# Optimization experiments

Hardware: AMD Instinct MI355X
Metric: run time of the kernel (lower is better)

Reference implementation:

```python
import jax, jax.numpy as jnp
import numpy as np

B, L, T = 32, 256, 32
V_SIZE, D, H = 30000, 300, 256


def _gru(x, h0, Wih, Whh, bih, bhh):
    # x: [B,S,D], h0: [B,H]; PyTorch GRU gate order: r, z, n
    xg = jnp.einsum('bsd,gd->bsg', x, Wih) + bih  # [B,S,3H]

    def step(h, xg_t):
        gh = jnp.einsum('bh,gh->bg', h, Whh) + bhh
        ir, iz, in_ = jnp.split(xg_t, 3, axis=-1)
        hr, hz, hn_ = jnp.split(gh, 3, axis=-1)
        r = jax.nn.sigmoid(ir + hr)
        z = jax.nn.sigmoid(iz + hz)
        n = jnp.tanh(in_ + r * hn_)
        h_new = (1.0 - z) * n + z * h
        return h_new, h_new

    h_last, outs = jax.lax.scan(step, h0, jnp.swapaxes(xg, 0, 1))
    return jnp.swapaxes(outs, 0, 1), h_last  # [B,S,H], [B,H]


def setup_inputs() -> dict:
    rng = np.random.default_rng(0)
    Xin = rng.integers(0, V_SIZE, (B, L)).astype(np.int64)
    # strictly increasing segment ends; starts = previous end + 1
    Yindex = np.stack([np.sort(rng.choice(L, T, replace=False)) for _ in range(B)]).astype(np.int64)
    Xindex = np.concatenate([np.zeros((B, 1), np.int64), Yindex[:, :-1] + 1], axis=1)
    lens = np.full((B,), L, np.int64)
    s = 0.05
    p = lambda *shape: jnp.asarray(rng.standard_normal(shape) * s, jnp.float32)
    return {
        'Xin': jnp.asarray(Xin), 'Xindex': jnp.asarray(Xindex),
        'Yindex': jnp.asarray(Yindex), 'lens': jnp.asarray(lens),
        'emb': jnp.asarray(rng.standard_normal((V_SIZE, D)) * 0.1, jnp.float32),
        'Wih_e': p(3 * H, D), 'Whh_e': p(3 * H, H), 'bih_e': p(3 * H), 'bhh_e': p(3 * H),
        'Wih_d': p(3 * H, D), 'Whh_d': p(3 * H, H), 'bih_d': p(3 * H), 'bhh_d': p(3 * H),
        'W1': p(H, H), 'W2': p(H, H), 'Vv': p(H),
    }


def reference(Xin, Xindex, Yindex, lens, emb, Wih_e, Whh_e, bih_e, bhh_e,
              Wih_d, Whh_d, bih_d, bhh_d, W1, W2, Vv):
    # pointerEncoder (isbanor=False, dropout=0, lens==L so packed == plain)
    X = emb[Xin]                                   # [B,L,D]
    h0 = jnp.zeros((Xin.shape[0], Whh_e.shape[1]), X.dtype)
    hn, h_end = _gru(X, h0, Wih_e, Whh_e, bih_e, bhh_e)  # [B,L,H],[B,H]
    # training_decoder, vectorized over batch and decode steps
    dec_tok = jnp.take_along_axis(Xin, Xindex, axis=1)   # token ids at segment starts
    dx = emb[dec_tok]                              # [B,T,D]
    dout, _ = _gru(dx, h_end, Wih_d, Whh_d, bih_d, bhh_d)  # [B,T,H]
    # pointerLayer: v = selu(V . selu(W1 en + W2 d)), masked log_softmax over [start, curL)
    WE = jnp.einsum('blh,kh->blk', hn, W1)         # [B,L,H]
    WD = jnp.einsum('bth,kh->btk', dout, W2)       # [B,T,H]
    s = jax.nn.selu(WE[:, None, :, :] + WD[:, :, None, :])  # [B,T,L,H]
    v = jax.nn.selu(jnp.einsum('btlh,h->btl', s, Vv))        # [B,T,L]
    pos = jnp.arange(hn.shape[1])
    mask = (pos[None, None, :] >= Xindex[:, :, None]) & (pos[None, None, :] < lens[:, None, None])
    logits = jnp.where(mask, v, -jnp.inf)
    logp = jax.nn.log_softmax(logits, axis=-1)
    tgt_logp = jnp.take_along_axis(logp, Yindex[:, :, None], axis=-1)[..., 0]  # [B,T]
    return -jnp.mean(tgt_logp)  # batch_loss / LoopN
```

## Files before the change

### kernel.cpp

```cpp
#include <hip/hip_runtime.h>
#include <hip/hip_bf16.h>
#include <stdint.h>

#define B_  32
#define L_  256
#define T_  32
#define D_  300
#define H_  256
#define G3  768

__device__ __forceinline__ int sdot4(uint32_t a, uint32_t b, int acc) {
#if defined(__has_builtin) && __has_builtin(__builtin_amdgcn_sdot4)
  return __builtin_amdgcn_sdot4((int)a, (int)b, acc, false);
#else
  const int a0 = (int)(signed char)(a & 0xff),  b0 = (int)(signed char)(b & 0xff);
  const int a1 = (int)(signed char)((a >> 8) & 0xff),  b1 = (int)(signed char)((b >> 8) & 0xff);
  const int a2 = (int)(signed char)((a >> 16) & 0xff), b2 = (int)(signed char)((b >> 16) & 0xff);
  const int a3 = (int)(signed char)(a >> 24),          b3 = (int)(signed char)(b >> 24);
  return acc + a0 * b0 + a1 * b1 + a2 * b2 + a3 * b3;
#endif
}

__device__ __forceinline__ float rcp_f(float x) { return __builtin_amdgcn_rcpf(x); }
__device__ __forceinline__ float sigmoid_f(float x) { return rcp_f(1.0f + __expf(-x)); }
__device__ __forceinline__ float tanh_f(float x) {
  float e2 = __expf(2.0f * x);
  return 1.0f - 2.0f * rcp_f(e2 + 1.0f);
}

__global__ __launch_bounds__(256)
void pack_whh_i8(const float* __restrict__ Whh, uint32_t* __restrict__ wQ,
                 float* __restrict__ sw) {
  const int row = blockIdx.x * 4 + (threadIdx.x >> 6);
  const int lane = threadIdx.x & 63;
  const float* wr = Whh + (long)row * H_;
  float m = 0.0f;
#pragma unroll
  for (int u = 0; u < 4; ++u) m = fmaxf(m, fabsf(wr[lane + 64 * u]));
  for (int off = 32; off > 0; off >>= 1) m = fmaxf(m, __shfl_xor(m, off, 64));
  const float inv = m > 0.0f ? 127.0f / m : 0.0f;
  if (lane == 0) sw[row] = m > 0.0f ? m / (127.0f * 127.0f) : 0.0f;
  uint32_t d = 0;
#pragma unroll
  for (int u = 0; u < 4; ++u) {
    int qv = __float2int_rn(wr[4 * lane + u] * inv);
    qv = qv > 127 ? 127 : (qv < -127 ? -127 : qv);
    d |= ((uint32_t)(qv & 0xff)) << (8 * u);
  }
  wQ[(((size_t)(lane >> 2) * G3 + row) << 2) + (lane & 3)] = d;
}

__global__ __launch_bounds__(256)
void quant_rows(const float* __restrict__ A, const int* __restrict__ rowidx,
                uint32_t* __restrict__ out, float* __restrict__ scale,
                int M, int K, int Kd) {
  const int row = blockIdx.x * 4 + (threadIdx.x >> 6);
  const int lane = threadIdx.x & 63;
  if (row >= M) return;
  const float* ar = A + (long)(rowidx ? rowidx[row] : row) * K;
  float m = 0.0f;
  for (int e = lane; e < K; e += 64) m = fmaxf(m, fabsf(ar[e]));
  for (int off = 32; off > 0; off >>= 1) m = fmaxf(m, __shfl_xor(m, off, 64));
  const float inv = m > 0.0f ? 127.0f / m : 0.0f;
  if (lane == 0) scale[row] = m * (1.0f / 127.0f);
  for (int kd = lane; kd < Kd; kd += 64) {
    uint32_t d = 0;
#pragma unroll
    for (int u = 0; u < 4; ++u) {
      const int e = 4 * kd + u;
      int qv = (e < K) ? __float2int_rn(ar[e] * inv) : 0;
      qv = qv > 127 ? 127 : (qv < -127 ? -127 : qv);
      d |= ((uint32_t)(qv & 0xff)) << (8 * u);
    }
    out[(long)row * Kd + kd] = d;
  }
}

__global__ void bias_combine(const float* __restrict__ bih, const float* __restrict__ bhh,
                             float* __restrict__ bsum) {
  const int i = blockIdx.x * 256 + threadIdx.x;
  float v = bih[i];
  if (i < 2 * H_) v += bhh[i];
  bsum[i] = v;
}

__global__ void gather_dtok(const int* __restrict__ Xin, const int* __restrict__ Xindex,
                            int* __restrict__ dtok) {
  const int i = blockIdx.x * 256 + threadIdx.x;
  const int b = i >> 5;
  dtok[i] = Xin[b * L_ + Xindex[i]];
}

template<bool TRANSP, bool BIAS>
__global__ __launch_bounds__(256)
void gemm_i8(const uint32_t* __restrict__ Aq, const float* __restrict__ sa,
             const uint32_t* __restrict__ Wq, const float* __restrict__ swc,
             const float* __restrict__ bias, float* __restrict__ C,
             int M, int N, int Kd) {
  __shared__ uint32_t As[8][68];
  __shared__ uint32_t Ws[8][68];
  const int tid = threadIdx.x;
  const int bm = blockIdx.x, bn = blockIdx.y;
  const int ty = tid >> 4, tx = tid & 15;
  const int srow = tid >> 2;
  const int skd = (tid & 3) << 1;
  const uint32_t* Arow = Aq + (long)(bm * 64 + srow) * Kd + skd;
  const uint32_t* Wrow = Wq + (long)(bn * 64 + srow) * Kd + skd;
  int acc[4][4] = {};
  for (int k0 = 0; k0 < Kd; k0 += 8) {
    const uint32_t a0 = Arow[k0], a1 = Arow[k0 + 1];
    const uint32_t w0 = Wrow[k0], w1 = Wrow[k0 + 1];
    __syncthreads();
    As[skd][srow] = a0; As[skd + 1][srow] = a1;
    Ws[skd][srow] = w0; Ws[skd + 1][srow] = w1;
    __syncthreads();
#pragma unroll
    for (int kd = 0; kd < 8; ++kd) {
      const uint4 a4 = *(const uint4*)&As[kd][ty << 2];
      const uint4 b4 = *(const uint4*)&Ws[kd][tx << 2];
      acc[0][0] = sdot4(a4.x, b4.x, acc[0][0]);
      acc[0][1] = sdot4(a4.x, b4.y, acc[0][1]);
      acc[0][2] = sdot4(a4.x, b4.z, acc[0][2]);
      acc[0][3] = sdot4(a4.x, b4.w, acc[0][3]);
      acc[1][0] = sdot4(a4.y, b4.x, acc[1][0]);
      acc[1][1] = sdot4(a4.y, b4.y, acc[1][1]);
      acc[1][2] = sdot4(a4.y, b4.z, acc[1][2]);
      acc[1][3] = sdot4(a4.y, b4.w, acc[1][3]);
      acc[2][0] = sdot4(a4.z, b4.x, acc[2][0]);
      acc[2][1] = sdot4(a4.z, b4.y, acc[2][1]);
      acc[2][2] = sdot4(a4.z, b4.z, acc[2][2]);
      acc[2][3] = sdot4(a4.z, b4.w, acc[2][3]);
      acc[3][0] = sdot4(a4.w, b4.x, acc[3][0]);
      acc[3][1] = sdot4(a4.w, b4.y, acc[3][1]);
      acc[3][2] = sdot4(a4.w, b4.z, acc[3][2]);
      acc[3][3] = sdot4(a4.w, b4.w, acc[3][3]);
    }
  }
#pragma unroll
  for (int i = 0; i < 4; ++i) {
    const int m = bm * 64 + (ty << 2) + i;
    const float sai = sa[m];
#pragma unroll
    for (int j = 0; j < 4; ++j) {
      const int n = bn * 64 + (tx << 2) + j;
      float v = (float)acc[i][j] * sai * swc[n];
      if (BIAS) v += bias[n];
      if (TRANSP) C[(((long)(m >> 8) * N + n) << 8) + (m & 255)] = v;
      else        C[(long)m * N + n] = v;
    }
  }
}


#define PIN4(v) asm volatile("" : "+v"(v.x), "+v"(v.y), "+v"(v.z), "+v"(v.w))
#define DOT4W(accv, wv, hp) { \
  accv = sdot4(wv.x, hp.x, accv); accv = sdot4(wv.y, hp.y, accv); \
  accv = sdot4(wv.z, hp.z, accv); accv = sdot4(wv.w, hp.w, accv); }

__global__ __launch_bounds__(1024)
void gru_seq(const float* __restrict__ xg, const uint4* __restrict__ wQv,
             const float* __restrict__ sw, const float* __restrict__ bhh,
             const float* __restrict__ h0, float* __restrict__ hout,
             float* __restrict__ hlast, int S) {
  const int b = blockIdx.x;
  const int tid = threadIdx.x;
  const int j = tid & 255;
  const int q = tid >> 8;
  const int c0 = q * 4;
  const int o_r0 = (c0 + 0) * G3 + j,        o_r1 = (c0 + 1) * G3 + j;
  const int o_z0 = o_r0 + H_,                o_z1 = o_r1 + H_;
  const int o_n0 = o_r0 + 2 * H_,            o_n1 = o_r1 + 2 * H_;
  uint4 wr2 = wQv[(c0 + 2) * G3 + j],          wr3 = wQv[(c0 + 3) * G3 + j];
  uint4 wz2 = wQv[(c0 + 2) * G3 + H_ + j],     wz3 = wQv[(c0 + 3) * G3 + H_ + j];
  uint4 wn2 = wQv[(c0 + 2) * G3 + 2 * H_ + j], wn3 = wQv[(c0 + 3) * G3 + 2 * H_ + j];
  PIN4(wr2); PIN4(wr3); PIN4(wz2); PIN4(wz3); PIN4(wn2); PIN4(wn3);
  __shared__ __align__(16) uint32_t h2[2][H_ / 4];
  __shared__ int part[3][4][H_];
  float bhn = 0.0f, h = 0.0f, swr = 0.0f, swz = 0.0f, swn = 0.0f;
  const float* xp = xg + (long)b * S * G3;
  float* hp_out = hout + (long)b * S * H_;
  if (q == 0) {
    bhn = bhh[2 * H_ + j];
    swr = sw[j]; swz = sw[H_ + j]; swn = sw[2 * H_ + j];
    h = h0 ? h0[b * H_ + j] : 0.0f;
    ((signed char*)h2[0])[j] = (signed char)__float2int_rn(h * 127.0f);
  }
  __syncthreads();
  for (int t = 0; t < S; ++t) {
    const uint4* hq = (const uint4*)h2[t & 1] + q * 4;
    int ar = 0, az = 0, an = 0;
    uint4 s0 = wQv[o_r0], s1 = wQv[o_r1];
    float xr = 0.0f, xz = 0.0f, xn = 0.0f;
    if (q == 0) { xr = xp[j]; xz = xp[H_ + j]; xn = xp[2 * H_ + j]; }
    const uint4 hp2 = hq[2], hp3 = hq[3];
    DOT4W(ar, wr2, hp2) DOT4W(ar, wr3, hp3)
    const uint4 hp0 = hq[0], hp1 = hq[1];
    DOT4W(ar, s0, hp0) DOT4W(ar, s1, hp1)
    __builtin_amdgcn_sched_barrier(0);
    s0 = wQv[o_z0]; s1 = wQv[o_z1];
    DOT4W(az, wz2, hp2) DOT4W(az, wz3, hp3)
    DOT4W(az, s0, hp0) DOT4W(az, s1, hp1)
    __builtin_amdgcn_sched_barrier(0);
    s0 = wQv[o_n0]; s1 = wQv[o_n1];
    DOT4W(an, wn2, hp2) DOT4W(an, wn3, hp3)
    DOT4W(an, s0, hp0) DOT4W(an, s1, hp1)
    if (q) { part[0][q][j] = ar; part[1][q][j] = az; part[2][q][j] = an; }
    __syncthreads();
    if (q == 0) {
      const float arf = (float)(ar + part[0][1][j] + part[0][2][j] + part[0][3][j]) * swr;
      const float azf = (float)(az + part[1][1][j] + part[1][2][j] + part[1][3][j]) * swz;
      const float anf = (float)(an + part[2][1][j] + part[2][2][j] + part[2][3][j]) * swn;
      const float r = sigmoid_f(xr + arf);
      const float z = sigmoid_f(xz + azf);
      const float n = tanh_f(xn + r * (anf + bhn));
      h = (1.0f - z) * n + z * h;
      hp_out[j] = h;
      ((signed char*)h2[(t & 1) ^ 1])[j] = (signed char)__float2int_rn(h * 127.0f);
    }
    xp += G3;
    hp_out += H_;
    __syncthreads();
  }
  if (q == 0 && hlast) hlast[b * H_ + j] = h;
}

__global__ __launch_bounds__(256)
void pointer_loss(const float* __restrict__ WEt, const float* __restrict__ WD,
                  const float* __restrict__ Vv,
                  const int* __restrict__ Xindex, const int* __restrict__ Yindex,
                  const int* __restrict__ lens, float* __restrict__ out) {
  const int t = blockIdx.x, b = blockIdx.y;
  const int l = threadIdx.x;
  __shared__ float wd_s[H_], vv_s[H_];
  __shared__ float rbuf[4], sbuf[4], vy_s;
  const int bt = b * T_ + t;
  wd_s[l] = WD[(long)bt * H_ + l];
  vv_s[l] = Vv[l] * 1.0507009873554805f;
  __syncthreads();
  const float* wet = WEt + (long)b * H_ * L_;
  const float alpha = 1.6732632423543772f;
  float acc = 0.0f;
#pragma unroll 4
  for (int hh = 0; hh < H_; ++hh) {
    const float xsum = wet[hh * L_ + l] + wd_s[hh];
    const float sneg = alpha * (__expf(xsum) - 1.0f);
    const float s = xsum > 0.0f ? xsum : sneg;
    acc = fmaf(s, vv_s[hh], acc);
  }
  float v;
  {
    const float sneg = alpha * (__expf(acc) - 1.0f);
    v = 1.0507009873554805f * (acc > 0.0f ? acc : sneg);
  }
  const int start = Xindex[bt];
  const int len = lens[b];
  const bool valid = (l >= start) && (l < len);
  const int y = Yindex[bt];
  if (l == y) vy_s = v;
  float m = valid ? v : -INFINITY;
  for (int off = 32; off > 0; off >>= 1) m = fmaxf(m, __shfl_xor(m, off, 64));
  const int wid = l >> 6, lane = l & 63;
  if (lane == 0) rbuf[wid] = m;
  __syncthreads();
  const float mx = fmaxf(fmaxf(rbuf[0], rbuf[1]), fmaxf(rbuf[2], rbuf[3]));
  float e = valid ? __expf(v - mx) : 0.0f;
  for (int off = 32; off > 0; off >>= 1) e += __shfl_xor(e, off, 64);
  if (lane == 0) sbuf[wid] = e;
  __syncthreads();
  if (l == 0) {
    const float sum = sbuf[0] + sbuf[1] + sbuf[2] + sbuf[3];
    atomicAdd(out, (mx + __logf(sum) - vy_s) * (1.0f / (B_ * T_)));
  }
}

extern "C" void kernel_launch(void* const* d_in, const int* in_sizes, int n_in,
                              void* d_out, int out_size, void* d_ws, size_t ws_size,
                              hipStream_t stream) {
  (void)in_sizes; (void)n_in; (void)out_size; (void)ws_size;
  const int*   Xin    = (const int*)d_in[0];
  const int*   Xindex = (const int*)d_in[1];
  const int*   Yindex = (const int*)d_in[2];
  const int*   lens   = (const int*)d_in[3];
  const float* emb    = (const float*)d_in[4];
  const float* Wih_e  = (const float*)d_in[5];
  const float* Whh_e  = (const float*)d_in[6];
  const float* bih_e  = (const float*)d_in[7];
  const float* bhh_e  = (const float*)d_in[8];
  const float* Wih_d  = (const float*)d_in[9];
  const float* Whh_d  = (const float*)d_in[10];
  const float* bih_d  = (const float*)d_in[11];
  const float* bhh_d  = (const float*)d_in[12];
  const float* W1     = (const float*)d_in[13];
  const float* W2     = (const float*)d_in[14];
  const float* Vv     = (const float*)d_in[15];

  char* p = (char*)d_ws;
  auto take = [&](size_t bytes) { void* q = (void*)p; p += (bytes + 255) & ~(size_t)255; return q; };
  uint32_t* wQ_e   = (uint32_t*)take((size_t)64 * G3 * 4);
  uint32_t* wQ_d   = (uint32_t*)take((size_t)64 * G3 * 4);
  float*    sw_e   = (float*)take((size_t)768 * 4);
  float*    sw_d   = (float*)take((size_t)768 * 4);
  uint32_t* WihQ_e = (uint32_t*)take((size_t)768 * 80 * 4);
  uint32_t* WihQ_d = (uint32_t*)take((size_t)768 * 80 * 4);
  float*    sWih_e = (float*)take((size_t)768 * 4);
  float*    sWih_d = (float*)take((size_t)768 * 4);
  uint32_t* W1q    = (uint32_t*)take((size_t)256 * 64 * 4);
  uint32_t* W2q    = (uint32_t*)take((size_t)256 * 64 * 4);
  float*    sW1    = (float*)take((size_t)256 * 4);
  float*    sW2    = (float*)take((size_t)256 * 4);
  float*    bsum_e = (float*)take((size_t)768 * 4);
  float*    bsum_d = (float*)take((size_t)768 * 4);
  int*      dtok   = (int*)take((size_t)1024 * 4);
  float*    xg_e   = (float*)take((size_t)8192 * 768 * 4);
  float*    xg_d   = (float*)take((size_t)1024 * 768 * 4);
  float*    hn     = (float*)take((size_t)8192 * 256 * 4);
  float*    hend   = (float*)take((size_t)8192 * 4);
  float*    hl_d   = (float*)take((size_t)8192 * 4);
  float*    doutb  = (float*)take((size_t)1024 * 256 * 4);
  float*    WDb    = (float*)take((size_t)1024 * 256 * 4);
  uint32_t* Aqe    = (uint32_t*)take((size_t)8192 * 80 * 4);
  float*    saAe   = (float*)take((size_t)8192 * 4);
  uint32_t* Aqd    = (uint32_t*)take((size_t)1024 * 80 * 4);
  float*    saAd   = (float*)take((size_t)1024 * 4);
  float*    WEt  = xg_e;
  uint32_t* hnq  = Aqe;
  float*    sahn = saAe;
  uint32_t* dq   = Aqd;
  float*    sad  = saAd;

  hipMemsetAsync(d_out, 0, sizeof(float), stream);

  hipLaunchKernelGGL(pack_whh_i8, dim3(192), dim3(256), 0, stream, Whh_e, wQ_e, sw_e);
  hipLaunchKernelGGL(pack_whh_i8, dim3(192), dim3(256), 0, stream, Whh_d, wQ_d, sw_d);
  hipLaunchKernelGGL(bias_combine, dim3(3), dim3(256), 0, stream, bih_e, bhh_e, bsum_e);
  hipLaunchKernelGGL(bias_combine, dim3(3), dim3(256), 0, stream, bih_d, bhh_d, bsum_d);
  hipLaunchKernelGGL(gather_dtok, dim3(4), dim3(256), 0, stream, Xin, Xindex, dtok);

  hipLaunchKernelGGL(quant_rows, dim3(192), dim3(256), 0, stream,
                     Wih_e, (const int*)nullptr, WihQ_e, sWih_e, 768, 300, 80);
  hipLaunchKernelGGL(quant_rows, dim3(192), dim3(256), 0, stream,
                     Wih_d, (const int*)nullptr, WihQ_d, sWih_d, 768, 300, 80);
  hipLaunchKernelGGL(quant_rows, dim3(64), dim3(256), 0, stream,
                     W1, (const int*)nullptr, W1q, sW1, 256, 256, 64);
  hipLaunchKernelGGL(quant_rows, dim3(64), dim3(256), 0, stream,
                     W2, (const int*)nullptr, W2q, sW2, 256, 256, 64);
  hipLaunchKernelGGL(quant_rows, dim3(2048), dim3(256), 0, stream,
                     emb, Xin, Aqe, saAe, 8192, 300, 80);
  hipLaunchKernelGGL(quant_rows, dim3(256), dim3(256), 0, stream,
                     emb, dtok, Aqd, saAd, 1024, 300, 80);

  hipLaunchKernelGGL((gemm_i8<false, true>), dim3(128, 12), dim3(256), 0, stream,
                     Aqe, saAe, WihQ_e, sWih_e, bsum_e, xg_e, 8192, 768, 80);
  hipLaunchKernelGGL((gemm_i8<false, true>), dim3(16, 12), dim3(256), 0, stream,
                     Aqd, saAd, WihQ_d, sWih_d, bsum_d, xg_d, 1024, 768, 80);

  hipLaunchKernelGGL(gru_seq, dim3(32), dim3(1024), 0, stream,
                     xg_e, (const uint4*)wQ_e, sw_e, bhh_e, (const float*)nullptr,
                     hn, hend, L_);
  hipLaunchKernelGGL(gru_seq, dim3(32), dim3(1024), 0, stream,
                     xg_d, (const uint4*)wQ_d, sw_d, bhh_d, hend, doutb, hl_d, T_);

  hipLaunchKernelGGL(quant_rows, dim3(2048), dim3(256), 0, stream,
                     hn, (const int*)nullptr, hnq, sahn, 8192, 256, 64);
  hipLaunchKernelGGL(quant_rows, dim3(256), dim3(256), 0, stream,
                     doutb, (const int*)nullptr, dq, sad, 1024, 256, 64);
  hipLaunchKernelGGL((gemm_i8<true, false>), dim3(128, 4), dim3(256), 0, stream,
                     hnq, sahn, W1q, sW1, (const float*)nullptr, WEt, 8192, 256, 64);
  hipLaunchKernelGGL((gemm_i8<false, false>), dim3(16, 4), dim3(256), 0, stream,
                     dq, sad, W2q, sW2, (const float*)nullptr, WDb, 1024, 256, 64);

  hipLaunchKernelGGL(pointer_loss, dim3(T_, B_), dim3(256), 0, stream,
                     WEt, WDb, Vv, Xindex, Yindex, lens, (float*)d_out);
}
```

Before: 342.5 us.

## Fuse prep kernels into one launch and broadcast GRU hidden state via readlane

Eleven small preprocessing launches (weight packing, quantization, bias combine, decoder token gather) are merged into one prep_all kernel, and the two post-GRU quantizations into one post_quant kernel, cutting launch overhead and the serialization between tiny kernels. In the recurrent GRU kernel, each thread keeps more of its int8 weights in registers (8 pinned uint4 instead of 6), so fewer weight loads are reissued per step. The hidden state is read once per lane from LDS and broadcast with readlane instead of vector LDS loads, and partial sums are exchanged as one int4 instead of three scalars. The extra pinned registers raise register pressure at 1024 threads per block.

After: 394.2 us. 1.15x slower.

```diff
diff --git a/kernel.cpp b/kernel.cpp
--- a/kernel.cpp
+++ b/kernel.cpp
@@ -28,10 +28,10 @@
   return 1.0f - 2.0f * rcp_f(e2 + 1.0f);
 }
 
-__global__ __launch_bounds__(256)
-void pack_whh_i8(const float* __restrict__ Whh, uint32_t* __restrict__ wQ,
-                 float* __restrict__ sw) {
-  const int row = blockIdx.x * 4 + (threadIdx.x >> 6);
+__device__ __forceinline__ void pack_body(int blk, const float* __restrict__ Whh,
+                                          uint32_t* __restrict__ wQ,
+                                          float* __restrict__ sw) {
+  const int row = blk * 4 + (threadIdx.x >> 6);
   const int lane = threadIdx.x & 63;
   const float* wr = Whh + (long)row * H_;
   float m = 0.0f;
@@ -50,14 +50,20 @@
   wQ[(((size_t)(lane >> 2) * G3 + row) << 2) + (lane & 3)] = d;
 }
 
-__global__ __launch_bounds__(256)
-void quant_rows(const float* __restrict__ A, const int* __restrict__ rowidx,
-                uint32_t* __restrict__ out, float* __restrict__ scale,
-                int M, int K, int Kd) {
-  const int row = blockIdx.x * 4 + (threadIdx.x >> 6);
+__device__ __forceinline__ void quant_body(int blk, const float* __restrict__ A,
+                                           const int* __restrict__ rowidx,
+                                           const int* __restrict__ Xin2,
+                                           const int* __restrict__ Xidx2,
+                                           uint32_t* __restrict__ out,
+                                           float* __restrict__ scale,
+                                           int M, int K, int Kd) {
+  const int row = blk * 4 + (threadIdx.x >> 6);
   const int lane = threadIdx.x & 63;
   if (row >= M) return;
-  const float* ar = A + (long)(rowidx ? rowidx[row] : row) * K;
+  long src = row;
+  if (rowidx) src = rowidx[row];
+  else if (Xin2) src = Xin2[(row >> 5) * L_ + Xidx2[row]];
+  const float* ar = A + src * (long)K;
   float m = 0.0f;
   for (int e = lane; e < K; e += 64) m = fmaxf(m, fabsf(ar[e]));
   for (int off = 32; off > 0; off >>= 1) m = fmaxf(m, __shfl_xor(m, off, 64));
@@ -76,19 +82,59 @@
   }
 }
 
-__global__ void bias_combine(const float* __restrict__ bih, const float* __restrict__ bhh,
-                             float* __restrict__ bsum) {
-  const int i = blockIdx.x * 256 + threadIdx.x;
-  float v = bih[i];
-  if (i < 2 * H_) v += bhh[i];
-  bsum[i] = v;
-}
-
-__global__ void gather_dtok(const int* __restrict__ Xin, const int* __restrict__ Xindex,
-                            int* __restrict__ dtok) {
-  const int i = blockIdx.x * 256 + threadIdx.x;
-  const int b = i >> 5;
-  dtok[i] = Xin[b * L_ + Xindex[i]];
+__global__ __launch_bounds__(256)
+void prep_all(const float* __restrict__ Whh_e, const float* __restrict__ Whh_d,
+              uint32_t* __restrict__ wQ_e, uint32_t* __restrict__ wQ_d,
+              float* __restrict__ sw_e, float* __restrict__ sw_d,
+              const float* __restrict__ Wih_e, const float* __restrict__ Wih_d,
+              uint32_t* __restrict__ WihQ_e, uint32_t* __restrict__ WihQ_d,
+              float* __restrict__ sWih_e, float* __restrict__ sWih_d,
+              const float* __restrict__ W1, const float* __restrict__ W2,
+              uint32_t* __restrict__ W1q, uint32_t* __restrict__ W2q,
+              float* __restrict__ sW1, float* __restrict__ sW2,
+              const float* __restrict__ emb, const int* __restrict__ Xin,
+              const int* __restrict__ Xindex,
+              uint32_t* __restrict__ Aqe, float* __restrict__ saAe,
+              uint32_t* __restrict__ Aqd, float* __restrict__ saAd,
+              const float* __restrict__ bih_e, const float* __restrict__ bhh_e,
+              float* __restrict__ bsum_e,
+              const float* __restrict__ bih_d, const float* __restrict__ bhh_d,
+              float* __restrict__ bsum_d) {
+  const int blk = blockIdx.x;
+  if (blk < 192)        pack_body(blk, Whh_e, wQ_e, sw_e);
+  else if (blk < 384)   pack_body(blk - 192, Whh_d, wQ_d, sw_d);
+  else if (blk < 576)   quant_body(blk - 384, Wih_e, nullptr, nullptr, nullptr,
+                                   WihQ_e, sWih_e, 768, 300, 80);
+  else if (blk < 768)   quant_body(blk - 576, Wih_d, nullptr, nullptr, nullptr,
+                                   WihQ_d, sWih_d, 768, 300, 80);
+  else if (blk < 832)   quant_body(blk - 768, W1, nullptr, nullptr, nullptr,
+                                   W1q, sW1, 256, 256, 64);
+  else if (blk < 896)   quant_body(blk - 832, W2, nullptr, nullptr, nullptr,
+                                   W2q, sW2, 256, 256, 64);
+  else if (blk < 2944)  quant_body(blk - 896, emb, Xin, nullptr, nullptr,
+                                   Aqe, saAe, 8192, 300, 80);
+  else if (blk < 3200)  quant_body(blk - 2944, emb, nullptr, Xin, Xindex,
+                                   Aqd, saAd, 1024, 300, 80);
+  else {
+    const int blk2 = blk - 3200;
+    const int i = (blk2 % 3) * 256 + threadIdx.x;
+    const float* bih = blk2 < 3 ? bih_e : bih_d;
+    const float* bhh = blk2 < 3 ? bhh_e : bhh_d;
+    float* bsum = blk2 < 3 ? bsum_e : bsum_d;
+    float v = bih[i];
+    if (i < 2 * H_) v += bhh[i];
+    bsum[i] = v;
+  }
+}
+
+__global__ __launch_bounds__(256)
+void post_quant(const float* __restrict__ hn, uint32_t* __restrict__ hnq,
+                float* __restrict__ sahn,
+                const float* __restrict__ doutb, uint32_t* __restrict__ dq,
+                float* __restrict__ sad) {
+  const int blk = blockIdx.x;
+  if (blk < 2048) quant_body(blk, hn, nullptr, nullptr, nullptr, hnq, sahn, 8192, 256, 64);
+  else            quant_body(blk - 2048, doutb, nullptr, nullptr, nullptr, dq, sad, 1024, 256, 64);
 }
 
 template<bool TRANSP, bool BIAS>
@@ -153,9 +199,9 @@
 
 
 #define PIN4(v) asm volatile("" : "+v"(v.x), "+v"(v.y), "+v"(v.z), "+v"(v.w))
-#define DOT4W(accv, wv, hp) { \
-  accv = sdot4(wv.x, hp.x, accv); accv = sdot4(wv.y, hp.y, accv); \
-  accv = sdot4(wv.z, hp.z, accv); accv = sdot4(wv.w, hp.w, accv); }
+#define DOTS(acc, wv_, ha, hb, hc, hd) { \
+  acc = sdot4(wv_.x, ha, acc); acc = sdot4(wv_.y, hb, acc); \
+  acc = sdot4(wv_.z, hc, acc); acc = sdot4(wv_.w, hd, acc); }
 
 __global__ __launch_bounds__(1024)
 void gru_seq(const float* __restrict__ xg, const uint4* __restrict__ wQv,
@@ -166,16 +212,25 @@
   const int tid = threadIdx.x;
   const int j = tid & 255;
   const int q = tid >> 8;
+  const int qb = q << 4;
   const int c0 = q * 4;
-  const int o_r0 = (c0 + 0) * G3 + j,        o_r1 = (c0 + 1) * G3 + j;
-  const int o_z0 = o_r0 + H_,                o_z1 = o_r1 + H_;
-  const int o_n0 = o_r0 + 2 * H_,            o_n1 = o_r1 + 2 * H_;
-  uint4 wr2 = wQv[(c0 + 2) * G3 + j],          wr3 = wQv[(c0 + 3) * G3 + j];
-  uint4 wz2 = wQv[(c0 + 2) * G3 + H_ + j],     wz3 = wQv[(c0 + 3) * G3 + H_ + j];
-  uint4 wn2 = wQv[(c0 + 2) * G3 + 2 * H_ + j], wn3 = wQv[(c0 + 3) * G3 + 2 * H_ + j];
-  PIN4(wr2); PIN4(wr3); PIN4(wz2); PIN4(wz3); PIN4(wn2); PIN4(wn3);
-  __shared__ __align__(16) uint32_t h2[2][H_ / 4];
-  __shared__ int part[3][4][H_];
+  const int o_r0 = (c0 + 0) * G3 + j;
+  const int o_z0 = o_r0 + H_;
+  const int o_n0 = o_r0 + 2 * H_;
+  const int o_n1 = (c0 + 1) * G3 + 2 * H_ + j;
+  uint4 wr1 = wQv[(c0 + 1) * G3 + j];
+  uint4 wr2 = wQv[(c0 + 2) * G3 + j];
+  uint4 wr3 = wQv[(c0 + 3) * G3 + j];
+  uint4 wz1 = wQv[(c0 + 1) * G3 + H_ + j];
+  uint4 wz2 = wQv[(c0 + 2) * G3 + H_ + j];
+  uint4 wz3 = wQv[(c0 + 3) * G3 + H_ + j];
+  uint4 wn2 = wQv[(c0 + 2) * G3 + 2 * H_ + j];
+  uint4 wn3 = wQv[(c0 + 3) * G3 + 2 * H_ + j];
+  PIN4(wr1); PIN4(wr2); PIN4(wr3);
+  PIN4(wz1); PIN4(wz2); PIN4(wz3);
+  PIN4(wn2); PIN4(wn3);
+  __shared__ uint32_t h2[2][64];
+  __shared__ int4 partv[4][H_];
   float bhn = 0.0f, h = 0.0f, swr = 0.0f, swz = 0.0f, swn = 0.0f;
   const float* xp = xg + (long)b * S * G3;
   float* hp_out = hout + (long)b * S * H_;
@@ -187,29 +242,51 @@
   }
   __syncthreads();
   for (int t = 0; t < S; ++t) {
-    const uint4* hq = (const uint4*)h2[t & 1] + q * 4;
-    int ar = 0, az = 0, an = 0;
-    uint4 s0 = wQv[o_r0], s1 = wQv[o_r1];
+    const uint32_t hv = h2[t & 1][tid & 63];
+    const uint4 sr  = wQv[o_r0];
+    const uint4 szc = wQv[o_z0];
+    const uint4 sn0 = wQv[o_n0];
+    const uint4 sn1 = wQv[o_n1];
     float xr = 0.0f, xz = 0.0f, xn = 0.0f;
     if (q == 0) { xr = xp[j]; xz = xp[H_ + j]; xn = xp[2 * H_ + j]; }
-    const uint4 hp2 = hq[2], hp3 = hq[3];
-    DOT4W(ar, wr2, hp2) DOT4W(ar, wr3, hp3)
-    const uint4 hp0 = hq[0], hp1 = hq[1];
-    DOT4W(ar, s0, hp0) DOT4W(ar, s1, hp1)
-    __builtin_amdgcn_sched_barrier(0);
-    s0 = wQv[o_z0]; s1 = wQv[o_z1];
-    DOT4W(az, wz2, hp2) DOT4W(az, wz3, hp3)
-    DOT4W(az, s0, hp0) DOT4W(az, s1, hp1)
-    __builtin_amdgcn_sched_barrier(0);
-    s0 = wQv[o_n0]; s1 = wQv[o_n1];
-    DOT4W(an, wn2, hp2) DOT4W(an, wn3, hp3)
-    DOT4W(an, s0, hp0) DOT4W(an, s1, hp1)
-    if (q) { part[0][q][j] = ar; part[1][q][j] = az; part[2][q][j] = an; }
+    const uint32_t hs0  = __builtin_amdgcn_readlane(hv, qb + 0);
+    const uint32_t hs1  = __builtin_amdgcn_readlane(hv, qb + 1);
+    const uint32_t hs2  = __builtin_amdgcn_readlane(hv, qb + 2);
+    const uint32_t hs3  = __builtin_amdgcn_readlane(hv, qb + 3);
+    const uint32_t hs4  = __builtin_amdgcn_readlane(hv, qb + 4);
+    const uint32_t hs5  = __builtin_amdgcn_readlane(hv, qb + 5);
+    const uint32_t hs6  = __builtin_amdgcn_readlane(hv, qb + 6);
+    const uint32_t hs7  = __builtin_amdgcn_readlane(hv, qb + 7);
+    const uint32_t hs8  = __builtin_amdgcn_readlane(hv, qb + 8);
+    const uint32_t hs9  = __builtin_amdgcn_readlane(hv, qb + 9);
+    const uint32_t hs10 = __builtin_amdgcn_readlane(hv, qb + 10);
+    const uint32_t hs11 = __builtin_amdgcn_readlane(hv, qb + 11);
+    const uint32_t hs12 = __builtin_amdgcn_readlane(hv, qb + 12);
+    const uint32_t hs13 = __builtin_amdgcn_readlane(hv, qb + 13);
+    const uint32_t hs14 = __builtin_amdgcn_readlane(hv, qb + 14);
+    const uint32_t hs15 = __builtin_amdgcn_readlane(hv, qb + 15);
+    int ar = 0, az = 0, an = 0;
+    DOTS(ar, wr1, hs4, hs5, hs6, hs7)
+    DOTS(ar, wr2, hs8, hs9, hs10, hs11)
+    DOTS(ar, wr3, hs12, hs13, hs14, hs15)
+    DOTS(az, wz1, hs4, hs5, hs6, hs7)
+    DOTS(az, wz2, hs8, hs9, hs10, hs11)
+    DOTS(az, wz3, hs12, hs13, hs14, hs15)
+    DOTS(an, wn2, hs8, hs9, hs10, hs11)
+    DOTS(an, wn3, hs12, hs13, hs14, hs15)
+    DOTS(ar, sr,  hs0, hs1, hs2, hs3)
+    DOTS(az, szc, hs0, hs1, hs2, hs3)
+    DOTS(an, sn0, hs0, hs1, hs2, hs3)
+    DOTS(an, sn1, hs4, hs5, hs6, hs7)
+    if (q) partv[q][j] = make_int4(ar, az, an, 0);
     __syncthreads();
     if (q == 0) {
-      const float arf = (float)(ar + part[0][1][j] + part[0][2][j] + part[0][3][j]) * swr;
-      const float azf = (float)(az + part[1][1][j] + part[1][2][j] + part[1][3][j]) * swz;
-      const float anf = (float)(an + part[2][1][j] + part[2][2][j] + part[2][3][j]) * swn;
+      const int4 p1 = partv[1][j];
+      const int4 p2 = partv[2][j];
+      const int4 p3 = partv[3][j];
+      const float arf = (float)(ar + p1.x + p2.x + p3.x) * swr;
+      const float azf = (float)(az + p1.y + p2.y + p3.y) * swz;
+      const float anf = (float)(an + p1.z + p2.z + p3.z) * swn;
       const float r = sigmoid_f(xr + arf);
       const float z = sigmoid_f(xz + azf);
       const float n = tanh_f(xn + r * (anf + bhn));
@@ -310,7 +387,6 @@
   float*    sW2    = (float*)take((size_t)256 * 4);
   float*    bsum_e = (float*)take((size_t)768 * 4);
   float*    bsum_d = (float*)take((size_t)768 * 4);
-  int*      dtok   = (int*)take((size_t)1024 * 4);
   float*    xg_e   = (float*)take((size_t)8192 * 768 * 4);
   float*    xg_d   = (float*)take((size_t)1024 * 768 * 4);
   float*    hn     = (float*)take((size_t)8192 * 256 * 4);
@@ -330,24 +406,12 @@
 
   hipMemsetAsync(d_out, 0, sizeof(float), stream);
 
-  hipLaunchKernelGGL(pack_whh_i8, dim3(192), dim3(256), 0, stream, Whh_e, wQ_e, sw_e);
-  hipLaunchKernelGGL(pack_whh_i8, dim3(192), dim3(256), 0, stream, Whh_d, wQ_d, sw_d);
-  hipLaunchKernelGGL(bias_combine, dim3(3), dim3(256), 0, stream, bih_e, bhh_e, bsum_e);
-  hipLaunchKernelGGL(bias_combine, dim3(3), dim3(256), 0, stream, bih_d, bhh_d, bsum_d);
-  hipLaunchKernelGGL(gather_dtok, dim3(4), dim3(256), 0, stream, Xin, Xindex, dtok);
-
-  hipLaunchKernelGGL(quant_rows, dim3(192), dim3(256), 0, stream,
-                     Wih_e, (const int*)nullptr, WihQ_e, sWih_e, 768, 300, 80);
-  hipLaunchKernelGGL(quant_rows, dim3(192), dim3(256), 0, stream,
-                     Wih_d, (const int*)nullptr, WihQ_d, sWih_d, 768, 300, 80);
-  hipLaunchKernelGGL(quant_rows, dim3(64), dim3(256), 0, stream,
-                     W1, (const int*)nullptr, W1q, sW1, 256, 256, 64);
-  hipLaunchKernelGGL(quant_rows, dim3(64), dim3(256), 0, stream,
-                     W2, (const int*)nullptr, W2q, sW2, 256, 256, 64);
-  hipLaunchKernelGGL(quant_rows, dim3(2048), dim3(256), 0, stream,
-                     emb, Xin, Aqe, saAe, 8192, 300, 80);
-  hipLaunchKernelGGL(quant_rows, dim3(256), dim3(256), 0, stream,
-                     emb, dtok, Aqd, saAd, 1024, 300, 80);
+  hipLaunchKernelGGL(prep_all, dim3(3206), dim3(256), 0, stream,
+                     Whh_e, Whh_d, wQ_e, wQ_d, sw_e, sw_d,
+                     Wih_e, Wih_d, WihQ_e, WihQ_d, sWih_e, sWih_d,
+                     W1, W2, W1q, W2q, sW1, sW2,
+                     emb, Xin, Xindex, Aqe, saAe, Aqd, saAd,
+                     bih_e, bhh_e, bsum_e, bih_d, bhh_d, bsum_d);
 
   hipLaunchKernelGGL((gemm_i8<false, true>), dim3(128, 12), dim3(256), 0, stream,
                      Aqe, saAe, WihQ_e, sWih_e, bsum_e, xg_e, 8192, 768, 80);
@@ -360,10 +424,9 @@
   hipLaunchKernelGGL(gru_seq, dim3(32), dim3(1024), 0, stream,
                      xg_d, (const uint4*)wQ_d, sw_d, bhh_d, hend, doutb, hl_d, T_);
 
-  hipLaunchKernelGGL(quant_rows, dim3(2048), dim3(256), 0, stream,
-                     hn, (const int*)nullptr, hnq, sahn, 8192, 256, 64);
-  hipLaunchKernelGGL(quant_rows, dim3(256), dim3(256), 0, stream,
-                     doutb, (const int*)nullptr, dq, sad, 1024, 256, 64);
+  hipLaunchKernelGGL(post_quant, dim3(2304), dim3(256), 0, stream,
+                     hn, hnq, sahn, doutb, dq, sad);
+
   hipLaunchKernelGGL((gemm_i8<true, false>), dim3(128, 4), dim3(256), 0, stream,
                      hnq, sahn, W1q, sW1, (const float*)nullptr, WEt, 8192, 256, 64);
   hipLaunchKernelGGL((gemm_i8<false, false>), dim3(16, 4), dim3(256), 0, stream,
```
